# Kernel optimization log

Measured on AMD Instinct MI355X. Metric: run time of the kernel, lower is better.

## Reference

```python
import jax, jax.numpy as jnp
import numpy as np
from jax import lax

# Module config (matches init_kwargs)
C_IN, C_OUT, D_STATE = 512, 256, 16
D_INNER = 2 * C_OUT          # canonical Mamba expand=2
DT_RANK = C_OUT // 16        # ceil(256/16) = 16
D_CONV = 4
BN_EPS = 1e-5


def setup_inputs() -> dict:
    key = jax.random.key(0)
    ks = jax.random.split(key, 16)
    s = 0.02
    B, H, W = 8, 64, 64
    inp = {
        "x": jax.random.normal(ks[0], (B, C_IN, H, W), jnp.float32),
        # lateral 1x1 conv
        "lateral_w": jax.random.normal(ks[1], (C_OUT, C_IN), jnp.float32) * s,
        "lateral_b": jnp.zeros((C_OUT,), jnp.float32),
        # mamba block params
        "in_proj_w": jax.random.normal(ks[2], (2 * D_INNER, C_OUT), jnp.float32) * s,
        "conv1d_w": jax.random.normal(ks[3], (D_INNER, D_CONV), jnp.float32) * s,
        "conv1d_b": jnp.zeros((D_INNER,), jnp.float32),
        "x_proj_w": jax.random.normal(ks[4], (DT_RANK + 2 * D_STATE, D_INNER), jnp.float32) * s,
        "dt_proj_w": jax.random.normal(ks[5], (D_INNER, DT_RANK), jnp.float32) * s,
        "dt_proj_b": jnp.full((D_INNER,), -4.0, jnp.float32),  # softplus -> small dt
        "A_log": jnp.log(jnp.broadcast_to(jnp.arange(1, D_STATE + 1, dtype=jnp.float32), (D_INNER, D_STATE))),  # S4D-real init
        "D_param": jnp.ones((D_INNER,), jnp.float32),
        "out_proj_w": jax.random.normal(ks[6], (C_OUT, D_INNER), jnp.float32) * s,
        # refine: 3x3 conv + BN (eval) + ReLU
        "refine_w": jax.random.normal(ks[7], (C_OUT, C_OUT, 3, 3), jnp.float32) * s,
        "refine_b": jnp.zeros((C_OUT,), jnp.float32),
        "bn_gamma": jnp.ones((C_OUT,), jnp.float32),
        "bn_beta": jnp.zeros((C_OUT,), jnp.float32),
        "bn_mean": jnp.zeros((C_OUT,), jnp.float32),
        "bn_var": jnp.ones((C_OUT,), jnp.float32),
    }
    return inp


def _silu(v):
    return v * jax.nn.sigmoid(v)


def _mamba(u, in_proj_w, conv1d_w, conv1d_b, x_proj_w, dt_proj_w, dt_proj_b,
           A_log, D_param, out_proj_w):
    """Canonical Mamba block on u: (B, L, D) -> (B, L, D)."""
    B, L, D = u.shape
    xz = jnp.einsum('bld,ed->ble', u, in_proj_w)            # (B,L,2*d_inner)
    xm, z = jnp.split(xz, 2, axis=-1)
    # causal depthwise conv1d over L
    xc = xm.transpose(0, 2, 1)                               # (B,d_inner,L)
    xc = lax.conv_general_dilated(xc, conv1d_w[:, None, :], (1,),
                                  [(D_CONV - 1, 0)],
                                  feature_group_count=D_INNER)
    xc = _silu(xc + conv1d_b[None, :, None]).transpose(0, 2, 1)  # (B,L,d_inner)
    proj = jnp.einsum('bld,ed->ble', xc, x_proj_w)           # (B,L,dt_rank+2*N)
    dt_r = proj[..., :DT_RANK]
    B_ssm = proj[..., DT_RANK:DT_RANK + D_STATE]             # (B,L,N)
    C_ssm = proj[..., DT_RANK + D_STATE:]                    # (B,L,N)
    dt = jax.nn.softplus(jnp.einsum('blr,dr->bld', dt_r, dt_proj_w) + dt_proj_b)
    A = -jnp.exp(A_log)                                      # (d_inner,N)

    def step(h, inputs):
        dt_t, B_t, C_t, x_t = inputs                         # (B,d), (B,N), (B,N), (B,d)
        dA = jnp.exp(dt_t[..., None] * A)                    # (B,d,N)
        h = dA * h + dt_t[..., None] * B_t[:, None, :] * x_t[..., None]
        y = jnp.einsum('bdn,bn->bd', h, C_t)
        return h, y

    xs = (dt.transpose(1, 0, 2), B_ssm.transpose(1, 0, 2),
          C_ssm.transpose(1, 0, 2), xc.transpose(1, 0, 2))
    h0 = jnp.zeros((B, D_INNER, D_STATE), u.dtype)
    _, ys = lax.scan(step, h0, xs)                           # (L,B,d_inner)
    y = ys.transpose(1, 0, 2) + xc * D_param
    y = y * _silu(z)
    return jnp.einsum('ble,de->bld', y, out_proj_w)          # (B,L,D)


def reference(x, lateral_w, lateral_b, in_proj_w, conv1d_w, conv1d_b, x_proj_w,
              dt_proj_w, dt_proj_b, A_log, D_param, out_proj_w, refine_w,
              refine_b, bn_gamma, bn_beta, bn_mean, bn_var):
    B, _, H, W = x.shape
    # lateral 1x1 conv
    xl = jnp.einsum('oi,bihw->bohw', lateral_w, x) + lateral_b[None, :, None, None]
    # mamba on flattened spatial sequence, residual add
    u = xl.reshape(B, C_OUT, H * W).transpose(0, 2, 1)        # (B,L,C)
    m = _mamba(u, in_proj_w, conv1d_w, conv1d_b, x_proj_w, dt_proj_w,
               dt_proj_b, A_log, D_param, out_proj_w)
    xr = xl + m.transpose(0, 2, 1).reshape(B, C_OUT, H, W)
    # refine: 3x3 conv + BN(eval) + ReLU
    r = lax.conv_general_dilated(xr, refine_w, (1, 1), [(1, 1), (1, 1)])
    r = r + refine_b[None, :, None, None]
    inv = bn_gamma / jnp.sqrt(bn_var + BN_EPS)
    r = (r - bn_mean[None, :, None, None]) * inv[None, :, None, None] + bn_beta[None, :, None, None]
    return jax.nn.relu(r)
```

## Files before the change

kernel.cpp:

```cpp
#include <hip/hip_runtime.h>
#include <math.h>

#define NB   8
#define CIN  512
#define COUT 256
#define DIN  512
#define LHW  4096
#define NCHK 128
#define CHL  32
#define PW   66
#define PPOS (PW*PW)

typedef __attribute__((ext_vector_type(8))) short bf16x8;
typedef __attribute__((ext_vector_type(4))) float f32x4;

__device__ __forceinline__ float siluf(float v)  { return v / (1.f + __expf(-v)); }
__device__ __forceinline__ float splusf(float v) {
  return fmaxf(v, 0.f) + __logf(1.f + __expf(-fabsf(v)));
}

__device__ __forceinline__ unsigned short f2b(float f) {
  union { float f; unsigned u; } v; v.f = f;
  unsigned r = v.u + 0x7fff + ((v.u >> 16) & 1);
  return (unsigned short)(r >> 16);
}
__device__ __forceinline__ float b2f(unsigned int u) {
  union { unsigned u; float f; } v; v.u = (u & 0xffffu) << 16; return v.f;
}

__device__ __forceinline__ void gload16(const unsigned short* g, unsigned short* l) {
  __builtin_amdgcn_global_load_lds(
      (const __attribute__((address_space(1))) unsigned int*)g,
      (__attribute__((address_space(3))) unsigned int*)l, 16, 0, 0);
}

#define WO1 131072
#define WO2 393216
#define WO3 425984
#define WO4 557056
#define WO5 1146880
__global__ __launch_bounds__(256)
void k_wprep(const float* __restrict__ lw, const float* __restrict__ ipw,
             const float* __restrict__ xpw, const float* __restrict__ opw,
             const float* __restrict__ rw, const float* __restrict__ dtpw,
             unsigned short* __restrict__ wb, unsigned short* __restrict__ wfb) {
  const int i = blockIdx.x * 256 + threadIdx.x;
  if (i < WO1)      wb[i] = f2b(lw[i]);
  else if (i < WO2) wb[i] = f2b(ipw[i - WO1]);
  else if (i < WO3) {
    const int j = i - WO2, row = j >> 9, col = j & 511;
    wb[i] = (row < 48) ? f2b(xpw[row * 512 + col]) : (unsigned short)0;
  }
  else if (i < WO4) wb[i] = f2b(opw[i - WO3]);
  else if (i < WO5) {
    const int j = i - WO4, o = j / 2304, kk = j % 2304;
    const int tap = kk >> 8, ch = kk & 255;
    wb[i] = f2b(rw[(o * 256 + ch) * 9 + tap]);
  }
  else {
    const int j = i - WO5, row = j >> 9, e = j & 511;
    float v = 0.f;
    if (row < 512) {
#pragma unroll
      for (int r = 0; r < 16; ++r)
        v = fmaf(dtpw[row * 16 + r], xpw[r * 512 + e], v);
    } else if (row < 560) {
      v = xpw[(row - 512) * 512 + e];
    }
    wfb[j] = f2b(v);
  }
}

__global__ __launch_bounds__(256)
void k_xpose(const float* __restrict__ x, unsigned short* __restrict__ xt) {
  __shared__ unsigned short Ts[64][80];
  const int b  = blockIdx.z;
  const int k0 = blockIdx.y * 64;
  const int l0 = blockIdx.x * 64;
  const int t  = threadIdx.x;
  const int tx = t & 15, ty = t >> 4;
#pragma unroll
  for (int r = 0; r < 4; ++r) {
    const int k = ty + r * 16;
    float4 v = *(const float4*)(x + ((size_t)b * CIN + k0 + k) * LHW + l0 + tx * 4);
    Ts[tx*4+0][k] = f2b(v.x);
    Ts[tx*4+1][k] = f2b(v.y);
    Ts[tx*4+2][k] = f2b(v.z);
    Ts[tx*4+3][k] = f2b(v.w);
  }
  __syncthreads();
  const int lr = t >> 2, kc = (t & 3) * 16;
  unsigned short* dst = xt + ((size_t)b * LHW + l0 + lr) * CIN + k0 + kc;
  *(uint4*)dst       = *(const uint4*)&Ts[lr][kc];
  *(uint4*)(dst + 8) = *(const uint4*)&Ts[lr][kc + 8];
}

template<int RSA, int RSB, int KTOT>
__device__ __forceinline__ void gemm_loop_128(
    const unsigned short* __restrict__ Ab, const unsigned short* __restrict__ Bb,
    unsigned short (&As)[2][4096], unsigned short (&Bs)[2][4096],
    int t, f32x4 acc[4][4]) {
  const int w = t >> 6, lane = t & 63;
  const int wm = w >> 1, wn = w & 1;
  const int arow = t >> 2;
  const int acol = (((t & 3) ^ ((t >> 3) & 3))) * 8;
  const int fr = lane & 15;
  const int g8 = ((lane >> 4) * 8) ^ (((fr >> 1) & 3) * 8);
  for (int k0 = 0; k0 < KTOT; k0 += 64) {
    __syncthreads();
    gload16(Ab + (size_t)arow * RSA + k0 + acol,             &As[0][w * 512]);
    gload16(Ab + (size_t)(64 + arow) * RSA + k0 + acol,      &As[0][2048 + w*512]);
    gload16(Bb + (size_t)arow * RSB + k0 + acol,             &Bs[0][w * 512]);
    gload16(Bb + (size_t)(64 + arow) * RSB + k0 + acol,      &Bs[0][2048 + w*512]);
    gload16(Ab + (size_t)arow * RSA + k0 + 32 + acol,        &As[1][w * 512]);
    gload16(Ab + (size_t)(64 + arow) * RSA + k0 + 32 + acol, &As[1][2048 + w*512]);
    gload16(Bb + (size_t)arow * RSB + k0 + 32 + acol,        &Bs[1][w * 512]);
    gload16(Bb + (size_t)(64 + arow) * RSB + k0 + 32 + acol, &Bs[1][2048 + w*512]);
    __syncthreads();
#pragma unroll
    for (int h = 0; h < 2; ++h) {
      bf16x8 af[4], bf[4];
#pragma unroll
      for (int f = 0; f < 4; ++f) {
        af[f] = *(const bf16x8*)&As[h][(wm*64 + f*16 + fr) * 32 + g8];
        bf[f] = *(const bf16x8*)&Bs[h][(wn*64 + f*16 + fr) * 32 + g8];
      }
#pragma unroll
      for (int i = 0; i < 4; ++i)
#pragma unroll
        for (int j = 0; j < 4; ++j)
          acc[i][j] = __builtin_amdgcn_mfma_f32_16x16x32_bf16(af[i], bf[j], acc[i][j], 0, 0, 0);
    }
  }
}

__global__ __launch_bounds__(256)
void k_lat_mfma(const unsigned short* __restrict__ xt, const unsigned short* __restrict__ lwb,
                const float* __restrict__ lb, unsigned short* __restrict__ ub) {
  __shared__ __align__(16) unsigned short As[2][4096], Bs[2][4096];
  const int t = threadIdx.x, lane = t & 63, w = t >> 6;
  const int wm = w >> 1, wn = w & 1;
  const int b = blockIdx.z, m0 = blockIdx.y * 128, n0 = blockIdx.x * 128;
  f32x4 acc[4][4] = {};
  gemm_loop_128<512, 512, 512>(xt + ((size_t)b * LHW + m0) * 512,
                               lwb + (size_t)n0 * 512, As, Bs, t, acc);
  const int fr = lane & 15, q4 = (lane >> 4) * 4;
#pragma unroll
  for (int i = 0; i < 4; ++i) {
    const int l = m0 + wm*64 + i*16 + q4;
#pragma unroll
    for (int j = 0; j < 4; ++j) {
      const int o = n0 + wn*64 + j*16 + fr;
      const float bias = lb[o];
      unsigned short* dst = ub + ((size_t)b * LHW + l) * COUT + o;
#pragma unroll
      for (int q = 0; q < 4; ++q)
        dst[(size_t)q * COUT] = f2b(acc[i][j][q] + bias);
    }
  }
}

__global__ __launch_bounds__(256)
void k_inproj_mfma(const unsigned short* __restrict__ ub, const unsigned short* __restrict__ ipwb,
                   unsigned short* __restrict__ xm_b, unsigned short* __restrict__ zsb) {
  __shared__ __align__(16) unsigned short As[2][4096], Bs[2][4096];
  const int t = threadIdx.x, lane = t & 63, w = t >> 6;
  const int wm = w >> 1, wn = w & 1;
  const int b = blockIdx.z, m0 = blockIdx.y * 128, n0 = blockIdx.x * 128;
  f32x4 acc[4][4] = {};
  gemm_loop_128<256, 256, 256>(ub + ((size_t)b * LHW + m0) * 256,
                               ipwb + (size_t)n0 * 256, As, Bs, t, acc);
  const int fr = lane & 15, q4 = (lane >> 4) * 4;
  const bool isz = (n0 >= 512);
#pragma unroll
  for (int i = 0; i < 4; ++i) {
    const int l = m0 + wm*64 + i*16 + q4;
#pragma unroll
    for (int j = 0; j < 4; ++j) {
      const int e = n0 + wn*64 + j*16 + fr;
      if (isz) {
        unsigned short* dst = zsb + ((size_t)b * LHW + l) * DIN + (e - 512);
#pragma unroll
        for (int q = 0; q < 4; ++q)
          dst[(size_t)q * DIN] = f2b(siluf(acc[i][j][q]));
      } else {
        unsigned short* dst = xm_b + ((size_t)b * LHW + l) * DIN + e;
#pragma unroll
        for (int q = 0; q < 4; ++q)
          dst[(size_t)q * DIN] = f2b(acc[i][j][q]);
      }
    }
  }
}

__global__ __launch_bounds__(256)
void k_conv1d(const unsigned short* __restrict__ xm_b, const float* __restrict__ cw,
              const float* __restrict__ cb, unsigned short* __restrict__ xc_b) {
  const int tid = blockIdx.x * 256 + threadIdx.x;
  const int e8 = tid & 63;
  const int lg = tid >> 6;
  const int l0 = (lg & 511) * 8;
  const int b  = lg >> 9;
  const int e0 = e8 * 8;
  float bias[8];
  *(float4*)&bias[0] = *(const float4*)(cb + e0);
  *(float4*)&bias[4] = *(const float4*)(cb + e0 + 4);
  float wv[8][4];
#pragma unroll
  for (int q = 0; q < 8; ++q) {
    float4 w4 = *(const float4*)(cw + (e0 + q) * 4);
    wv[q][0] = w4.x; wv[q][1] = w4.y; wv[q][2] = w4.z; wv[q][3] = w4.w;
  }
  const unsigned short* base = xm_b + ((size_t)b * LHW + l0) * DIN + e0;
  uint4 rows[11];
  const uint4 z4 = make_uint4(0u, 0u, 0u, 0u);
#pragma unroll
  for (int r = 0; r < 11; ++r) {
    const int ll = r - 3;
    rows[r] = (l0 + ll >= 0) ? *(const uint4*)(base + (ptrdiff_t)ll * DIN) : z4;
  }
  unsigned short* outb = xc_b + ((size_t)b * LHW + l0) * DIN + e0;
#pragma unroll
  for (int j = 0; j < 8; ++j) {
    float acc[8];
#pragma unroll
    for (int q = 0; q < 8; ++q) acc[q] = bias[q];
#pragma unroll
    for (int k = 0; k < 4; ++k) {
      const uint4 raw = rows[j + k];
      acc[0] = fmaf(b2f(raw.x),       wv[0][k], acc[0]);
      acc[1] = fmaf(b2f(raw.x >> 16), wv[1][k], acc[1]);
      acc[2] = fmaf(b2f(raw.y),       wv[2][k], acc[2]);
      acc[3] = fmaf(b2f(raw.y >> 16), wv[3][k], acc[3]);
      acc[4] = fmaf(b2f(raw.z),       wv[4][k], acc[4]);
      acc[5] = fmaf(b2f(raw.z >> 16), wv[5][k], acc[5]);
      acc[6] = fmaf(b2f(raw.w),       wv[6][k], acc[6]);
      acc[7] = fmaf(b2f(raw.w >> 16), wv[7][k], acc[7]);
    }
    uint4 o;
    o.x = (unsigned)f2b(siluf(acc[0])) | ((unsigned)f2b(siluf(acc[1])) << 16);
    o.y = (unsigned)f2b(siluf(acc[2])) | ((unsigned)f2b(siluf(acc[3])) << 16);
    o.z = (unsigned)f2b(siluf(acc[4])) | ((unsigned)f2b(siluf(acc[5])) << 16);
    o.w = (unsigned)f2b(siluf(acc[6])) | ((unsigned)f2b(siluf(acc[7])) << 16);
    *(uint4*)(outb + (size_t)j * DIN) = o;
  }
}

__global__ __launch_bounds__(256)
void k_xdt_mfma(const unsigned short* __restrict__ xc_b, const unsigned short* __restrict__ wfb,
                const float* __restrict__ dtpb,
                unsigned short* __restrict__ dtb, float* __restrict__ proj) {
  __shared__ __align__(16) unsigned short As[2][4096], Bs[2][4096];
  const int t = threadIdx.x, lane = t & 63, w = t >> 6;
  const int wm = w >> 1, wn = w & 1;
  const int b = blockIdx.z, m0 = blockIdx.x * 128, n0 = blockIdx.y * 128;
  f32x4 acc[4][4] = {};
  gemm_loop_128<512, 512, 512>(xc_b + ((size_t)b * LHW + m0) * 512,
                               wfb + (size_t)n0 * 512, As, Bs, t, acc);
  const int fr = lane & 15, q4 = (lane >> 4) * 4;
#pragma unroll
  for (int i = 0; i < 4; ++i) {
    const int l = m0 + wm*64 + i*16 + q4;
#pragma unroll
    for (int j = 0; j < 4; ++j) {
      const int c = n0 + wn*64 + j*16 + fr;
      if (c < 512) {
        const float bias = dtpb[c];
        unsigned short* dst = dtb + ((size_t)b * LHW + l) * 512 + c;
#pragma unroll
        for (int q = 0; q < 4; ++q)
          dst[(size_t)q * 512] = f2b(splusf(acc[i][j][q] + bias));
      } else if (c < 560) {
        float* dst = proj + ((size_t)b * LHW + l) * 48 + (c - 512);
#pragma unroll
        for (int q = 0; q < 4; ++q)
          dst[(size_t)q * 48] = acc[i][j][q];
      }
    }
  }
}

__global__ __launch_bounds__(512, 4)
void k_scanA(const float* __restrict__ proj, const unsigned short* __restrict__ dtb,
             const unsigned short* __restrict__ xc_b,
             const float* __restrict__ A_log, float* __restrict__ PS) {
  __shared__ float prs[CHL * 16];
  const int bx = blockIdx.x;
  const int b = bx >> 7, c = bx & 127;
  const int d = threadIdx.x;
  const size_t rbase = (size_t)b * LHW + c * CHL;
  for (int i = d; i < CHL * 4; i += 512) {
    const int row = i >> 2, c4 = i & 3;
    *(float4*)&prs[row * 16 + c4 * 4] = *(const float4*)(proj + (rbase + row) * 48 + 16 + c4 * 4);
  }
  float An[16], h[16];
#pragma unroll
  for (int q = 0; q < 4; ++q) {
    float4 a4 = *(const float4*)(A_log + d*16 + q*4);
    An[q*4+0] = -__expf(a4.x); An[q*4+1] = -__expf(a4.y);
    An[q*4+2] = -__expf(a4.z); An[q*4+3] = -__expf(a4.w);
  }
#pragma unroll
  for (int n = 0; n < 16; ++n) h[n] = 0.f;
  const float An0 = An[0];
  bool lin = true;
#pragma unroll
  for (int n = 1; n < 16; ++n)
    lin = lin && (fabsf(An[n] - (n + 1) * An0) <= 1e-4f * fabsf(An[n]));
  float sdt = 0.f;
  const unsigned short* dt0 = dtb + rbase * 512 + d;
  const unsigned short* xc0 = xc_b + rbase * DIN + d;
  __syncthreads();
  for (int i = 0; i < CHL; ++i) {
    const float dt = b2f(dt0[(size_t)i * 512]);
    sdt += dt;
    const float dtx = dt * b2f(xc0[(size_t)i * DIN]);
    float dA[16];
    if (lin) {
      const float e1 = __expf(dt * An0);
      const float e2 = e1 * e1, e3 = e2 * e1, e4 = e2 * e2;
      dA[0] = e1; dA[1] = e2; dA[2] = e3; dA[3] = e4;
#pragma unroll
      for (int n = 4; n < 16; ++n) dA[n] = dA[n-4] * e4;
    } else {
#pragma unroll
      for (int n = 0; n < 16; ++n) dA[n] = __expf(dt * An[n]);
    }
    const float* pr = &prs[i * 16];
#pragma unroll
    for (int q = 0; q < 4; ++q) {
      float4 B4 = *(const float4*)(pr + q*4);
      h[q*4+0] = fmaf(dA[q*4+0], h[q*4+0], dtx * B4.x);
      h[q*4+1] = fmaf(dA[q*4+1], h[q*4+1], dtx * B4.y);
      h[q*4+2] = fmaf(dA[q*4+2], h[q*4+2], dtx * B4.z);
      h[q*4+3] = fmaf(dA[q*4+3], h[q*4+3], dtx * B4.w);
    }
  }
  float* o = PS + ((size_t)bx * 512 + d) * 32;
#pragma unroll
  for (int q = 0; q < 4; ++q)
    *(float4*)(o + q*4) = make_float4(__expf(sdt*An[q*4+0]), __expf(sdt*An[q*4+1]),
                                      __expf(sdt*An[q*4+2]), __expf(sdt*An[q*4+3]));
#pragma unroll
  for (int q = 0; q < 4; ++q)
    *(float4*)(o + 16 + q*4) = make_float4(h[q*4], h[q*4+1], h[q*4+2], h[q*4+3]);
}

__global__ __launch_bounds__(256)
void k_scanB(const float* __restrict__ PS, float* __restrict__ hst) {
  const int tid = blockIdx.x * 256 + threadIdx.x;
  const int n = tid & 15;
  const int d = (tid >> 4) & 511;
  const int b = tid >> 13;
  float h = 0.f;
  for (int c = 0; c < NCHK; ++c) {
    const size_t idx = (size_t)((b*NCHK + c)*512 + d);
    hst[idx*16 + n] = h;
    h = PS[idx*32 + n] * h + PS[idx*32 + 16 + n];
  }
}

__global__ __launch_bounds__(512, 4)
void k_scanC(const float* __restrict__ proj, const unsigned short* __restrict__ dtb,
             const unsigned short* __restrict__ xc_b,
             const unsigned short* __restrict__ zsb, const float* __restrict__ hst,
             const float* __restrict__ A_log, const float* __restrict__ Dpar,
             unsigned short* __restrict__ ydata) {
  __shared__ float prs[CHL * 32];
  const int bx = blockIdx.x;
  const int b = bx >> 7, c = bx & 127;
  const int d = threadIdx.x;
  const size_t rbase = (size_t)b * LHW + c * CHL;
  for (int i = d; i < CHL * 8; i += 512) {
    const int row = i >> 3, c4 = i & 7;
    *(float4*)&prs[row * 32 + c4 * 4] = *(const float4*)(proj + (rbase + row) * 48 + 16 + c4 * 4);
  }
  float An[16], h[16];
#pragma unroll
  for (int q = 0; q < 4; ++q) {
    float4 a4 = *(const float4*)(A_log + d*16 + q*4);
    An[q*4+0] = -__expf(a4.x); An[q*4+1] = -__expf(a4.y);
    An[q*4+2] = -__expf(a4.z); An[q*4+3] = -__expf(a4.w);
  }
#pragma unroll
  for (int q = 0; q < 4; ++q) {
    float4 h4 = *(const float4*)(hst + ((size_t)bx * 512 + d) * 16 + q*4);
    h[q*4+0] = h4.x; h[q*4+1] = h4.y; h[q*4+2] = h4.z; h[q*4+3] = h4.w;
  }
  const float An0 = An[0];
  bool lin = true;
#pragma unroll
  for (int n = 1; n < 16; ++n)
    lin = lin && (fabsf(An[n] - (n + 1) * An0) <= 1e-4f * fabsf(An[n]));
  const float dp = Dpar[d];
  const unsigned short* dt0 = dtb + rbase * 512 + d;
  const unsigned short* xc0 = xc_b + rbase * DIN + d;
  const unsigned short* zs0 = zsb + rbase * DIN + d;
  unsigned short* y0 = ydata + rbase * DIN + d;
  __syncthreads();
  for (int i = 0; i < CHL; ++i) {
    const float dt = b2f(dt0[(size_t)i * 512]);
    const float xt = b2f(xc0[(size_t)i * DIN]);
    const float zv = b2f(zs0[(size_t)i * DIN]);
    const float dtx = dt * xt;
    float dA[16];
    if (lin) {
      const float e1 = __expf(dt * An0);
      const float e2 = e1 * e1, e3 = e2 * e1, e4 = e2 * e2;
      dA[0] = e1; dA[1] = e2; dA[2] = e3; dA[3] = e4;
#pragma unroll
      for (int n = 4; n < 16; ++n) dA[n] = dA[n-4] * e4;
    } else {
#pragma unroll
      for (int n = 0; n < 16; ++n) dA[n] = __expf(dt * An[n]);
    }
    const float* pr = &prs[i * 32];
    float y0a = 0.f, y1a = 0.f, y2a = 0.f, y3a = 0.f;
#pragma unroll
    for (int q = 0; q < 4; ++q) {
      float4 B4 = *(const float4*)(pr + q*4);
      float4 C4 = *(const float4*)(pr + 16 + q*4);
      h[q*4+0] = fmaf(dA[q*4+0], h[q*4+0], dtx * B4.x);
      h[q*4+1] = fmaf(dA[q*4+1], h[q*4+1], dtx * B4.y);
      h[q*4+2] = fmaf(dA[q*4+2], h[q*4+2], dtx * B4.z);
      h[q*4+3] = fmaf(dA[q*4+3], h[q*4+3], dtx * B4.w);
      y0a = fmaf(h[q*4+0], C4.x, y0a);
      y1a = fmaf(h[q*4+1], C4.y, y1a);
      y2a = fmaf(h[q*4+2], C4.z, y2a);
      y3a = fmaf(h[q*4+3], C4.w, y3a);
    }
    const float y = (y0a + y1a) + (y2a + y3a);
    y0[(size_t)i * DIN] = f2b((y + xt * dp) * zv);
  }
}

__global__ __launch_bounds__(256)
void k_outproj_mfma(const unsigned short* __restrict__ ydata, const unsigned short* __restrict__ opwb,
                    const unsigned short* __restrict__ ub, unsigned short* __restrict__ xrp) {
  __shared__ __align__(16) unsigned short As[2][4096], Bs[2][4096];
  const int t = threadIdx.x, lane = t & 63, w = t >> 6;
  const int wm = w >> 1, wn = w & 1;
  const int b = blockIdx.z, m0 = blockIdx.y * 128, n0 = blockIdx.x * 128;
  f32x4 acc[4][4] = {};
  gemm_loop_128<512, 512, 512>(ydata + ((size_t)b * LHW + m0) * 512,
                               opwb + (size_t)n0 * 512, As, Bs, t, acc);
  const int fr = lane & 15, q4 = (lane >> 4) * 4;
#pragma unroll
  for (int i = 0; i < 4; ++i) {
    const int lbase = m0 + wm*64 + i*16 + q4;
#pragma unroll
    for (int q = 0; q < 4; ++q) {
      const int l = lbase + q;
      const int pos = ((l >> 6) + 1) * PW + (l & 63) + 1;
#pragma unroll
      for (int j = 0; j < 4; ++j) {
        const int o = n0 + wn*64 + j*16 + fr;
        const float r = b2f(ub[((size_t)b * LHW + l) * COUT + o]);
        xrp[((size_t)b * PPOS + pos) * COUT + o] = f2b(acc[i][j][q] + r);
      }
    }
  }
}

__global__ __launch_bounds__(256)
void k_refine_mfma(const unsigned short* __restrict__ Aw,
                   const unsigned short* __restrict__ xrp,
                   const float* __restrict__ rb, const float* __restrict__ bng,
                   const float* __restrict__ bnb, const float* __restrict__ bnm,
                   const float* __restrict__ bnv, float* __restrict__ out) {
  __shared__ __align__(16) unsigned short As[4][4096], Bs[4][4096];
  const int t = threadIdx.x;
  const int lane = t & 63;
  const int w = t >> 6;
  const int wm = w >> 1, wn = w & 1;
  const int b  = blockIdx.z;
  const int m0 = blockIdx.y * 128;
  const int n0 = blockIdx.x * 128;
  const int y0 = n0 >> 6;
  const unsigned short* xb = xrp + (size_t)b * PPOS * COUT;
  const int arow = t >> 2;
  const int acol = (((t & 3) ^ ((t >> 3) & 3))) * 8;
  const int fr = lane & 15;
  const int g8 = ((lane >> 4) * 8) ^ (((fr >> 1) & 3) * 8);

#define RF_STAGE(ks, buf) {                                                            \
    const int tap_ = (ks) >> 3;                                                        \
    const int i0_  = ((ks) & 7) * 32;                                                  \
    const int ky_  = tap_ / 3, kx_ = tap_ - ky_ * 3;                                   \
    const int k0_  = tap_ * 256 + i0_;                                                 \
    const unsigned short* ga_ = Aw + (size_t)(m0 + arow) * 2304 + k0_ + acol;          \
    const unsigned short* gb_ = xb + ((size_t)((y0 + ky_) * PW + kx_ + arow)) * COUT + i0_ + acol; \
    gload16(ga_,              &As[buf][w * 512]);                                      \
    gload16(ga_ + 64 * 2304,  &As[buf][2048 + w * 512]);                               \
    gload16(gb_,              &Bs[buf][w * 512]);                                      \
    gload16(gb_ + PW * COUT,  &Bs[buf][2048 + w * 512]);                               \
  }

  f32x4 acc[4][4] = {};
  for (int ks = 0; ks < 72; ks += 4) {
    __syncthreads();
    RF_STAGE(ks, 0);
    RF_STAGE(ks + 1, 1);
    RF_STAGE(ks + 2, 2);
    RF_STAGE(ks + 3, 3);
    __syncthreads();
#pragma unroll
    for (int h = 0; h < 4; ++h) {
      bf16x8 af[4], bfr[4];
#pragma unroll
      for (int f = 0; f < 4; ++f) {
        af[f]  = *(const bf16x8*)&As[h][(wm*64 + f*16 + fr) * 32 + g8];
        bfr[f] = *(const bf16x8*)&Bs[h][(wn*64 + f*16 + fr) * 32 + g8];
      }
#pragma unroll
      for (int i = 0; i < 4; ++i)
#pragma unroll
        for (int j = 0; j < 4; ++j)
          acc[i][j] = __builtin_amdgcn_mfma_f32_16x16x32_bf16(af[i], bfr[j], acc[i][j], 0, 0, 0);
    }
  }
#undef RF_STAGE
  const int q4 = (lane >> 4) * 4;
#pragma unroll
  for (int i = 0; i < 4; ++i) {
    const int obase = m0 + wm*64 + i*16 + q4;
#pragma unroll
    for (int q = 0; q < 4; ++q) {
      const int o = obase + q;
      const float inv = bng[o] * rsqrtf(bnv[o] + 1e-5f);
      const float sh  = (rb[o] - bnm[o]) * inv + bnb[o];
      float* orow = out + ((size_t)b * COUT + o) * LHW + n0 + wn*64 + fr;
#pragma unroll
      for (int j = 0; j < 4; ++j)
        orow[j*16] = fmaxf(fmaf(acc[i][j][q], inv, sh), 0.f);
    }
  }
}

extern "C" void kernel_launch(void* const* d_in, const int* in_sizes, int n_in,
                              void* d_out, int out_size, void* d_ws, size_t ws_size,
                              hipStream_t stream) {
  const float* x    = (const float*)d_in[0];
  const float* lw   = (const float*)d_in[1];
  const float* lb   = (const float*)d_in[2];
  const float* ipw  = (const float*)d_in[3];
  const float* cw   = (const float*)d_in[4];
  const float* cb   = (const float*)d_in[5];
  const float* xpw  = (const float*)d_in[6];
  const float* dtpw = (const float*)d_in[7];
  const float* dtpb = (const float*)d_in[8];
  const float* Alog = (const float*)d_in[9];
  const float* Dpar = (const float*)d_in[10];
  const float* opw  = (const float*)d_in[11];
  const float* rw   = (const float*)d_in[12];
  const float* rb   = (const float*)d_in[13];
  const float* bng  = (const float*)d_in[14];
  const float* bnb  = (const float*)d_in[15];
  const float* bnm  = (const float*)d_in[16];
  const float* bnv  = (const float*)d_in[17];
  float* out = (float*)d_out;

  float* ws = (float*)d_ws;
  unsigned short* ub   = (unsigned short*)ws;
  unsigned short* xt   = (unsigned short*)(ws + 4194304);
  unsigned short* xm_b = (unsigned short*)(ws + 12582912);
  unsigned short* xc_b = (unsigned short*)(ws + 20971520);
  unsigned short* zsb  = (unsigned short*)(ws + 29360128);
  float* proj = ws + 37748736;
  float* PS   = ws + 39321600;
  float* hst  = ws + 56098816;
  unsigned short* wb  = (unsigned short*)(ws + 64487424);
  unsigned short* wfb = (unsigned short*)(ws + 65060864);
  unsigned short* lwb  = wb;
  unsigned short* ipwb = wb + WO1;
  unsigned short* opwb = wb + WO3;
  unsigned short* Aw   = wb + WO4;
  unsigned short* ydata = xm_b;
  unsigned short* dtb   = xt;
  unsigned short* xrp   = xt;

  k_wprep<<<dim3(5760), 256, 0, stream>>>(lw, ipw, xpw, opw, rw, dtpw, wb, wfb);
  k_xpose<<<dim3(64, 8, 8), 256, 0, stream>>>(x, xt);
  k_lat_mfma<<<dim3(2, 32, 8), 256, 0, stream>>>(xt, lwb, lb, ub);
  k_inproj_mfma<<<dim3(8, 32, 8), 256, 0, stream>>>(ub, ipwb, xm_b, zsb);
  k_conv1d<<<dim3(1024), 256, 0, stream>>>(xm_b, cw, cb, xc_b);
  k_xdt_mfma<<<dim3(32, 5, 8), 256, 0, stream>>>(xc_b, wfb, dtpb, dtb, proj);
  k_scanA<<<dim3(NB * NCHK), 512, 0, stream>>>(proj, dtb, xc_b, Alog, PS);
  k_scanB<<<dim3(256), 256, 0, stream>>>(PS, hst);
  k_scanC<<<dim3(NB * NCHK), 512, 0, stream>>>(proj, dtb, xc_b, zsb, hst, Alog, Dpar, ydata);
  hipMemsetAsync(xrp, 0, (size_t)NB * PPOS * COUT * sizeof(unsigned short), stream);
  k_outproj_mfma<<<dim3(2, 32, 8), 256, 0, stream>>>(ydata, opwb, ub, xrp);
  k_refine_mfma<<<dim3(32, 2, 8), 256, 0, stream>>>(Aw, xrp, rb, bng, bnb, bnm, bnv, out);
}
```

Measured before the change: 344.6 us.

## Split scan state across thread pairs and recompute chunk decay in scanB

The chunked selective-scan kernels now assign each channel to two threads, each holding eight of the sixteen state elements, with twice as many blocks. In scanC the partial output dot products are combined with a lane shuffle and only one thread of each pair writes. scanA no longer stores the per-chunk decay products; it stores only the chunk's summed dt, and scanB recomputes the decay with an exp, which roughly halves that intermediate's traffic. The aim is more parallelism and lower register pressure in the sequential scan, in exchange for duplicated dt/x/z loads per pair and extra shuffles.

```diff
diff --git a/kernel.cpp b/kernel.cpp
--- a/kernel.cpp
+++ b/kernel.cpp
@@ -282,31 +282,34 @@
 
 __global__ __launch_bounds__(512, 4)
 void k_scanA(const float* __restrict__ proj, const unsigned short* __restrict__ dtb,
-             const unsigned short* __restrict__ xc_b,
-             const float* __restrict__ A_log, float* __restrict__ PS) {
+             const unsigned short* __restrict__ xc_b, const float* __restrict__ A_log,
+             float* __restrict__ Sst, float* __restrict__ SDT) {
   __shared__ float prs[CHL * 16];
-  const int bx = blockIdx.x;
-  const int b = bx >> 7, c = bx & 127;
-  const int d = threadIdx.x;
+  const int chunkid = blockIdx.x >> 1;
+  const int dg = blockIdx.x & 1;
+  const int b = chunkid >> 7, c = chunkid & 127;
+  const int t = threadIdx.x;
+  const int d = dg * 256 + (t >> 1);
+  const int hf = t & 1;
   const size_t rbase = (size_t)b * LHW + c * CHL;
-  for (int i = d; i < CHL * 4; i += 512) {
+  for (int i = t; i < CHL * 4; i += 512) {
     const int row = i >> 2, c4 = i & 3;
     *(float4*)&prs[row * 16 + c4 * 4] = *(const float4*)(proj + (rbase + row) * 48 + 16 + c4 * 4);
   }
-  float An[16], h[16];
-#pragma unroll
-  for (int q = 0; q < 4; ++q) {
-    float4 a4 = *(const float4*)(A_log + d*16 + q*4);
-    An[q*4+0] = -__expf(a4.x); An[q*4+1] = -__expf(a4.y);
-    An[q*4+2] = -__expf(a4.z); An[q*4+3] = -__expf(a4.w);
-  }
-#pragma unroll
-  for (int n = 0; n < 16; ++n) h[n] = 0.f;
-  const float An0 = An[0];
+  float An[8], h[8];
+  {
+    float4 a0 = *(const float4*)(A_log + d*16 + hf*8);
+    float4 a1 = *(const float4*)(A_log + d*16 + hf*8 + 4);
+    An[0]=-__expf(a0.x); An[1]=-__expf(a0.y); An[2]=-__expf(a0.z); An[3]=-__expf(a0.w);
+    An[4]=-__expf(a1.x); An[5]=-__expf(a1.y); An[6]=-__expf(a1.z); An[7]=-__expf(a1.w);
+  }
+  const float An0g = -__expf(A_log[d * 16]);
+#pragma unroll
+  for (int k = 0; k < 8; ++k) h[k] = 0.f;
   bool lin = true;
 #pragma unroll
-  for (int n = 1; n < 16; ++n)
-    lin = lin && (fabsf(An[n] - (n + 1) * An0) <= 1e-4f * fabsf(An[n]));
+  for (int k = 0; k < 8; ++k)
+    lin = lin && (fabsf(An[k] - (hf*8 + k + 1) * An0g) <= 1e-4f * fabsf(An[k]));
   float sdt = 0.f;
   const unsigned short* dt0 = dtb + rbase * 512 + d;
   const unsigned short* xc0 = xc_b + rbase * DIN + d;
@@ -315,48 +318,45 @@
     const float dt = b2f(dt0[(size_t)i * 512]);
     sdt += dt;
     const float dtx = dt * b2f(xc0[(size_t)i * DIN]);
-    float dA[16];
+    float dA[8];
     if (lin) {
-      const float e1 = __expf(dt * An0);
-      const float e2 = e1 * e1, e3 = e2 * e1, e4 = e2 * e2;
-      dA[0] = e1; dA[1] = e2; dA[2] = e3; dA[3] = e4;
-#pragma unroll
-      for (int n = 4; n < 16; ++n) dA[n] = dA[n-4] * e4;
+      const float e1 = __expf(dt * An0g);
+      const float e2 = e1*e1, e3 = e2*e1, e4 = e2*e2;
+      const float e8 = e4*e4;
+      const float st = e1 * (hf ? e8 : 1.f);
+      dA[0]=st; dA[1]=st*e1; dA[2]=st*e2; dA[3]=st*e3;
+      dA[4]=dA[0]*e4; dA[5]=dA[1]*e4; dA[6]=dA[2]*e4; dA[7]=dA[3]*e4;
     } else {
 #pragma unroll
-      for (int n = 0; n < 16; ++n) dA[n] = __expf(dt * An[n]);
-    }
-    const float* pr = &prs[i * 16];
-#pragma unroll
-    for (int q = 0; q < 4; ++q) {
-      float4 B4 = *(const float4*)(pr + q*4);
-      h[q*4+0] = fmaf(dA[q*4+0], h[q*4+0], dtx * B4.x);
-      h[q*4+1] = fmaf(dA[q*4+1], h[q*4+1], dtx * B4.y);
-      h[q*4+2] = fmaf(dA[q*4+2], h[q*4+2], dtx * B4.z);
-      h[q*4+3] = fmaf(dA[q*4+3], h[q*4+3], dtx * B4.w);
-    }
-  }
-  float* o = PS + ((size_t)bx * 512 + d) * 32;
-#pragma unroll
-  for (int q = 0; q < 4; ++q)
-    *(float4*)(o + q*4) = make_float4(__expf(sdt*An[q*4+0]), __expf(sdt*An[q*4+1]),
-                                      __expf(sdt*An[q*4+2]), __expf(sdt*An[q*4+3]));
-#pragma unroll
-  for (int q = 0; q < 4; ++q)
-    *(float4*)(o + 16 + q*4) = make_float4(h[q*4], h[q*4+1], h[q*4+2], h[q*4+3]);
-}
-
-__global__ __launch_bounds__(256)
-void k_scanB(const float* __restrict__ PS, float* __restrict__ hst) {
+      for (int k = 0; k < 8; ++k) dA[k] = __expf(dt * An[k]);
+    }
+    const float* pr = &prs[i * 16 + hf * 8];
+    float4 B0 = *(const float4*)pr;
+    float4 B1 = *(const float4*)(pr + 4);
+    h[0]=fmaf(dA[0],h[0],dtx*B0.x); h[1]=fmaf(dA[1],h[1],dtx*B0.y);
+    h[2]=fmaf(dA[2],h[2],dtx*B0.z); h[3]=fmaf(dA[3],h[3],dtx*B0.w);
+    h[4]=fmaf(dA[4],h[4],dtx*B1.x); h[5]=fmaf(dA[5],h[5],dtx*B1.y);
+    h[6]=fmaf(dA[6],h[6],dtx*B1.z); h[7]=fmaf(dA[7],h[7],dtx*B1.w);
+  }
+  float* o = Sst + ((size_t)chunkid * 512 + d) * 16 + hf * 8;
+  *(float4*)o       = make_float4(h[0], h[1], h[2], h[3]);
+  *(float4*)(o + 4) = make_float4(h[4], h[5], h[6], h[7]);
+  if (!hf) SDT[(size_t)chunkid * 512 + d] = sdt;
+}
+
+__global__ __launch_bounds__(256)
+void k_scanB(const float* __restrict__ Sst, const float* __restrict__ SDT,
+             const float* __restrict__ A_log, float* __restrict__ hst) {
   const int tid = blockIdx.x * 256 + threadIdx.x;
   const int n = tid & 15;
   const int d = (tid >> 4) & 511;
   const int b = tid >> 13;
+  const float An = -__expf(A_log[d * 16 + n]);
   float h = 0.f;
   for (int c = 0; c < NCHK; ++c) {
     const size_t idx = (size_t)((b*NCHK + c)*512 + d);
     hst[idx*16 + n] = h;
-    h = PS[idx*32 + n] * h + PS[idx*32 + 16 + n];
+    h = __expf(SDT[idx] * An) * h + Sst[idx*16 + n];
   }
 }
 
@@ -367,31 +367,36 @@
              const float* __restrict__ A_log, const float* __restrict__ Dpar,
              unsigned short* __restrict__ ydata) {
   __shared__ float prs[CHL * 32];
-  const int bx = blockIdx.x;
-  const int b = bx >> 7, c = bx & 127;
-  const int d = threadIdx.x;
+  const int chunkid = blockIdx.x >> 1;
+  const int dg = blockIdx.x & 1;
+  const int b = chunkid >> 7, c = chunkid & 127;
+  const int t = threadIdx.x;
+  const int d = dg * 256 + (t >> 1);
+  const int hf = t & 1;
   const size_t rbase = (size_t)b * LHW + c * CHL;
-  for (int i = d; i < CHL * 8; i += 512) {
+  for (int i = t; i < CHL * 8; i += 512) {
     const int row = i >> 3, c4 = i & 7;
     *(float4*)&prs[row * 32 + c4 * 4] = *(const float4*)(proj + (rbase + row) * 48 + 16 + c4 * 4);
   }
-  float An[16], h[16];
-#pragma unroll
-  for (int q = 0; q < 4; ++q) {
-    float4 a4 = *(const float4*)(A_log + d*16 + q*4);
-    An[q*4+0] = -__expf(a4.x); An[q*4+1] = -__expf(a4.y);
-    An[q*4+2] = -__expf(a4.z); An[q*4+3] = -__expf(a4.w);
-  }
-#pragma unroll
-  for (int q = 0; q < 4; ++q) {
-    float4 h4 = *(const float4*)(hst + ((size_t)bx * 512 + d) * 16 + q*4);
-    h[q*4+0] = h4.x; h[q*4+1] = h4.y; h[q*4+2] = h4.z; h[q*4+3] = h4.w;
-  }
-  const float An0 = An[0];
+  float An[8], h[8];
+  {
+    float4 a0 = *(const float4*)(A_log + d*16 + hf*8);
+    float4 a1 = *(const float4*)(A_log + d*16 + hf*8 + 4);
+    An[0]=-__expf(a0.x); An[1]=-__expf(a0.y); An[2]=-__expf(a0.z); An[3]=-__expf(a0.w);
+    An[4]=-__expf(a1.x); An[5]=-__expf(a1.y); An[6]=-__expf(a1.z); An[7]=-__expf(a1.w);
+  }
+  const float An0g = -__expf(A_log[d * 16]);
+  {
+    const float* hsrc = hst + ((size_t)chunkid * 512 + d) * 16 + hf * 8;
+    float4 h0 = *(const float4*)hsrc;
+    float4 h1 = *(const float4*)(hsrc + 4);
+    h[0]=h0.x; h[1]=h0.y; h[2]=h0.z; h[3]=h0.w;
+    h[4]=h1.x; h[5]=h1.y; h[6]=h1.z; h[7]=h1.w;
+  }
   bool lin = true;
 #pragma unroll
-  for (int n = 1; n < 16; ++n)
-    lin = lin && (fabsf(An[n] - (n + 1) * An0) <= 1e-4f * fabsf(An[n]));
+  for (int k = 0; k < 8; ++k)
+    lin = lin && (fabsf(An[k] - (hf*8 + k + 1) * An0g) <= 1e-4f * fabsf(An[k]));
   const float dp = Dpar[d];
   const unsigned short* dt0 = dtb + rbase * 512 + d;
   const unsigned short* xc0 = xc_b + rbase * DIN + d;
@@ -403,34 +408,38 @@
     const float xt = b2f(xc0[(size_t)i * DIN]);
     const float zv = b2f(zs0[(size_t)i * DIN]);
     const float dtx = dt * xt;
-    float dA[16];
+    float dA[8];
     if (lin) {
-      const float e1 = __expf(dt * An0);
-      const float e2 = e1 * e1, e3 = e2 * e1, e4 = e2 * e2;
-      dA[0] = e1; dA[1] = e2; dA[2] = e3; dA[3] = e4;
-#pragma unroll
-      for (int n = 4; n < 16; ++n) dA[n] = dA[n-4] * e4;
+      const float e1 = __expf(dt * An0g);
+      const float e2 = e1*e1, e3 = e2*e1, e4 = e2*e2;
+      const float e8 = e4*e4;
+      const float st = e1 * (hf ? e8 : 1.f);
+      dA[0]=st; dA[1]=st*e1; dA[2]=st*e2; dA[3]=st*e3;
+      dA[4]=dA[0]*e4; dA[5]=dA[1]*e4; dA[6]=dA[2]*e4; dA[7]=dA[3]*e4;
     } else {
 #pragma unroll
-      for (int n = 0; n < 16; ++n) dA[n] = __expf(dt * An[n]);
+      for (int k = 0; k < 8; ++k) dA[k] = __expf(dt * An[k]);
     }
     const float* pr = &prs[i * 32];
-    float y0a = 0.f, y1a = 0.f, y2a = 0.f, y3a = 0.f;
-#pragma unroll
-    for (int q = 0; q < 4; ++q) {
-      float4 B4 = *(const float4*)(pr + q*4);
-      float4 C4 = *(const float4*)(pr + 16 + q*4);
-      h[q*4+0] = fmaf(dA[q*4+0], h[q*4+0], dtx * B4.x);
-      h[q*4+1] = fmaf(dA[q*4+1], h[q*4+1], dtx * B4.y);
-      h[q*4+2] = fmaf(dA[q*4+2], h[q*4+2], dtx * B4.z);
-      h[q*4+3] = fmaf(dA[q*4+3], h[q*4+3], dtx * B4.w);
-      y0a = fmaf(h[q*4+0], C4.x, y0a);
-      y1a = fmaf(h[q*4+1], C4.y, y1a);
-      y2a = fmaf(h[q*4+2], C4.z, y2a);
-      y3a = fmaf(h[q*4+3], C4.w, y3a);
-    }
-    const float y = (y0a + y1a) + (y2a + y3a);
-    y0[(size_t)i * DIN] = f2b((y + xt * dp) * zv);
+    float4 B0 = *(const float4*)(pr + hf * 8);
+    float4 B1 = *(const float4*)(pr + hf * 8 + 4);
+    float4 C0 = *(const float4*)(pr + 16 + hf * 8);
+    float4 C1 = *(const float4*)(pr + 16 + hf * 8 + 4);
+    float ya = 0.f, yb = 0.f;
+    h[0]=fmaf(dA[0],h[0],dtx*B0.x); ya=fmaf(h[0],C0.x,ya);
+    h[1]=fmaf(dA[1],h[1],dtx*B0.y); yb=fmaf(h[1],C0.y,yb);
+    h[2]=fmaf(dA[2],h[2],dtx*B0.z); ya=fmaf(h[2],C0.z,ya);
+    h[3]=fmaf(dA[3],h[3],dtx*B0.w); yb=fmaf(h[3],C0.w,yb);
+    h[4]=fmaf(dA[4],h[4],dtx*B1.x); ya=fmaf(h[4],C1.x,ya);
+    h[5]=fmaf(dA[5],h[5],dtx*B1.y); yb=fmaf(h[5],C1.y,yb);
+    h[6]=fmaf(dA[6],h[6],dtx*B1.z); ya=fmaf(h[6],C1.z,ya);
+    h[7]=fmaf(dA[7],h[7],dtx*B1.w); yb=fmaf(h[7],C1.w,yb);
+    float y = ya + yb;
+    y += __shfl_xor(y, 1);
+    if (!hf) {
+      const float ov = (y + xt * dp) * zv;
+      y0[(size_t)i * DIN] = f2b(ov);
+    }
   }
 }
 
@@ -567,8 +576,9 @@
   unsigned short* xc_b = (unsigned short*)(ws + 20971520);
   unsigned short* zsb  = (unsigned short*)(ws + 29360128);
   float* proj = ws + 37748736;
-  float* PS   = ws + 39321600;
-  float* hst  = ws + 56098816;
+  float* Sst  = ws + 39321600;
+  float* SDT  = ws + 47710208;
+  float* hst  = ws + 48234496;
   unsigned short* wb  = (unsigned short*)(ws + 64487424);
   unsigned short* wfb = (unsigned short*)(ws + 65060864);
   unsigned short* lwb  = wb;
@@ -585,9 +595,9 @@
   k_inproj_mfma<<<dim3(8, 32, 8), 256, 0, stream>>>(ub, ipwb, xm_b, zsb);
   k_conv1d<<<dim3(1024), 256, 0, stream>>>(xm_b, cw, cb, xc_b);
   k_xdt_mfma<<<dim3(32, 5, 8), 256, 0, stream>>>(xc_b, wfb, dtpb, dtb, proj);
-  k_scanA<<<dim3(NB * NCHK), 512, 0, stream>>>(proj, dtb, xc_b, Alog, PS);
-  k_scanB<<<dim3(256), 256, 0, stream>>>(PS, hst);
-  k_scanC<<<dim3(NB * NCHK), 512, 0, stream>>>(proj, dtb, xc_b, zsb, hst, Alog, Dpar, ydata);
+  k_scanA<<<dim3(NB * NCHK * 2), 512, 0, stream>>>(proj, dtb, xc_b, Alog, Sst, SDT);
+  k_scanB<<<dim3(256), 256, 0, stream>>>(Sst, SDT, Alog, hst);
+  k_scanC<<<dim3(NB * NCHK * 2), 512, 0, stream>>>(proj, dtb, xc_b, zsb, hst, Alog, Dpar, ydata);
   hipMemsetAsync(xrp, 0, (size_t)NB * PPOS * COUT * sizeof(unsigned short), stream);
   k_outproj_mfma<<<dim3(2, 32, 8), 256, 0, stream>>>(ydata, opwb, ub, xrp);
   k_refine_mfma<<<dim3(32, 2, 8), 256, 0, stream>>>(Aw, xrp, rb, bng, bnb, bnm, bnv, out);
```

Result: no change. 349.0 us (+1.3%).

## Use packed FP32 math in scan kernels and store chunk dt-sums instead of decay

Applied to the files above, without the earlier changes.

The scan recurrences in scanA and scanC now use v_pk_fma_f32/v_pk_mul_f32 inline asm on float pairs, roughly halving the VALU instruction count for the 16-state update and output dot product. scanA no longer writes per-chunk decay factors; it stores only the chunk dt sum, and scanB recomputes exp(sdt*A) itself. This cuts scanA's global write traffic and PS buffer size. In exchange scanB does an extra exp per step, and the inline asm may limit compiler scheduling.

```diff
diff --git a/kernel.cpp b/kernel.cpp
--- a/kernel.cpp
+++ b/kernel.cpp
@@ -13,6 +13,7 @@
 
 typedef __attribute__((ext_vector_type(8))) short bf16x8;
 typedef __attribute__((ext_vector_type(4))) float f32x4;
+typedef __attribute__((ext_vector_type(2))) float f32x2;
 
 __device__ __forceinline__ float siluf(float v)  { return v / (1.f + __expf(-v)); }
 __device__ __forceinline__ float splusf(float v) {
@@ -26,6 +27,17 @@
 }
 __device__ __forceinline__ float b2f(unsigned int u) {
   union { unsigned u; float f; } v; v.u = (u & 0xffffu) << 16; return v.f;
+}
+
+__device__ __forceinline__ f32x2 pk_fma(f32x2 a, f32x2 b, f32x2 c) {
+  f32x2 d;
+  asm("v_pk_fma_f32 %0, %1, %2, %3" : "=v"(d) : "v"(a), "v"(b), "v"(c));
+  return d;
+}
+__device__ __forceinline__ f32x2 pk_mul(f32x2 a, f32x2 b) {
+  f32x2 d;
+  asm("v_pk_mul_f32 %0, %1, %2" : "=v"(d) : "v"(a), "v"(b));
+  return d;
 }
 
 __device__ __forceinline__ void gload16(const unsigned short* g, unsigned short* l) {
@@ -282,8 +294,8 @@
 
 __global__ __launch_bounds__(512, 4)
 void k_scanA(const float* __restrict__ proj, const unsigned short* __restrict__ dtb,
-             const unsigned short* __restrict__ xc_b,
-             const float* __restrict__ A_log, float* __restrict__ PS) {
+             const unsigned short* __restrict__ xc_b, const float* __restrict__ A_log,
+             float* __restrict__ Sst, float* __restrict__ SDT) {
   __shared__ float prs[CHL * 16];
   const int bx = blockIdx.x;
   const int b = bx >> 7, c = bx & 127;
@@ -293,15 +305,16 @@
     const int row = i >> 2, c4 = i & 3;
     *(float4*)&prs[row * 16 + c4 * 4] = *(const float4*)(proj + (rbase + row) * 48 + 16 + c4 * 4);
   }
-  float An[16], h[16];
+  float An[16];
 #pragma unroll
   for (int q = 0; q < 4; ++q) {
     float4 a4 = *(const float4*)(A_log + d*16 + q*4);
     An[q*4+0] = -__expf(a4.x); An[q*4+1] = -__expf(a4.y);
     An[q*4+2] = -__expf(a4.z); An[q*4+3] = -__expf(a4.w);
   }
-#pragma unroll
-  for (int n = 0; n < 16; ++n) h[n] = 0.f;
+  f32x2 h2[8];
+#pragma unroll
+  for (int k = 0; k < 8; ++k) h2[k] = (f32x2){0.f, 0.f};
   const float An0 = An[0];
   bool lin = true;
 #pragma unroll
@@ -315,48 +328,50 @@
     const float dt = b2f(dt0[(size_t)i * 512]);
     sdt += dt;
     const float dtx = dt * b2f(xc0[(size_t)i * DIN]);
-    float dA[16];
+    const f32x2 dtx2 = (f32x2){dtx, dtx};
+    f32x2 dA2[8];
     if (lin) {
       const float e1 = __expf(dt * An0);
-      const float e2 = e1 * e1, e3 = e2 * e1, e4 = e2 * e2;
-      dA[0] = e1; dA[1] = e2; dA[2] = e3; dA[3] = e4;
-#pragma unroll
-      for (int n = 4; n < 16; ++n) dA[n] = dA[n-4] * e4;
+      const float e2 = e1*e1, e3 = e2*e1, e4 = e2*e2, e8 = e4*e4;
+      const f32x2 e4v = (f32x2){e4, e4}, e8v = (f32x2){e8, e8};
+      dA2[0] = (f32x2){e1, e2};
+      dA2[1] = (f32x2){e3, e4};
+      dA2[2] = pk_mul(dA2[0], e4v);
+      dA2[3] = pk_mul(dA2[1], e4v);
+      dA2[4] = pk_mul(dA2[0], e8v);
+      dA2[5] = pk_mul(dA2[1], e8v);
+      dA2[6] = pk_mul(dA2[2], e8v);
+      dA2[7] = pk_mul(dA2[3], e8v);
     } else {
 #pragma unroll
-      for (int n = 0; n < 16; ++n) dA[n] = __expf(dt * An[n]);
-    }
-    const float* pr = &prs[i * 16];
-#pragma unroll
-    for (int q = 0; q < 4; ++q) {
-      float4 B4 = *(const float4*)(pr + q*4);
-      h[q*4+0] = fmaf(dA[q*4+0], h[q*4+0], dtx * B4.x);
-      h[q*4+1] = fmaf(dA[q*4+1], h[q*4+1], dtx * B4.y);
-      h[q*4+2] = fmaf(dA[q*4+2], h[q*4+2], dtx * B4.z);
-      h[q*4+3] = fmaf(dA[q*4+3], h[q*4+3], dtx * B4.w);
-    }
-  }
-  float* o = PS + ((size_t)bx * 512 + d) * 32;
-#pragma unroll
-  for (int q = 0; q < 4; ++q)
-    *(float4*)(o + q*4) = make_float4(__expf(sdt*An[q*4+0]), __expf(sdt*An[q*4+1]),
-                                      __expf(sdt*An[q*4+2]), __expf(sdt*An[q*4+3]));
-#pragma unroll
-  for (int q = 0; q < 4; ++q)
-    *(float4*)(o + 16 + q*4) = make_float4(h[q*4], h[q*4+1], h[q*4+2], h[q*4+3]);
-}
-
-__global__ __launch_bounds__(256)
-void k_scanB(const float* __restrict__ PS, float* __restrict__ hst) {
+      for (int k = 0; k < 8; ++k)
+        dA2[k] = (f32x2){__expf(dt * An[2*k]), __expf(dt * An[2*k+1])};
+    }
+    const f32x2* B2 = (const f32x2*)&prs[i * 16];
+#pragma unroll
+    for (int k = 0; k < 8; ++k)
+      h2[k] = pk_fma(dA2[k], h2[k], pk_mul(dtx2, B2[k]));
+  }
+  float* o = Sst + ((size_t)bx * 512 + d) * 16;
+#pragma unroll
+  for (int k = 0; k < 4; ++k)
+    *(float4*)(o + k*4) = make_float4(h2[2*k].x, h2[2*k].y, h2[2*k+1].x, h2[2*k+1].y);
+  SDT[(size_t)bx * 512 + d] = sdt;
+}
+
+__global__ __launch_bounds__(256)
+void k_scanB(const float* __restrict__ Sst, const float* __restrict__ SDT,
+             const float* __restrict__ A_log, float* __restrict__ hst) {
   const int tid = blockIdx.x * 256 + threadIdx.x;
   const int n = tid & 15;
   const int d = (tid >> 4) & 511;
   const int b = tid >> 13;
+  const float An = -__expf(A_log[d * 16 + n]);
   float h = 0.f;
   for (int c = 0; c < NCHK; ++c) {
     const size_t idx = (size_t)((b*NCHK + c)*512 + d);
     hst[idx*16 + n] = h;
-    h = PS[idx*32 + n] * h + PS[idx*32 + 16 + n];
+    h = __expf(SDT[idx] * An) * h + Sst[idx*16 + n];
   }
 }
 
@@ -375,17 +390,19 @@
     const int row = i >> 3, c4 = i & 7;
     *(float4*)&prs[row * 32 + c4 * 4] = *(const float4*)(proj + (rbase + row) * 48 + 16 + c4 * 4);
   }
-  float An[16], h[16];
+  float An[16];
 #pragma unroll
   for (int q = 0; q < 4; ++q) {
     float4 a4 = *(const float4*)(A_log + d*16 + q*4);
     An[q*4+0] = -__expf(a4.x); An[q*4+1] = -__expf(a4.y);
     An[q*4+2] = -__expf(a4.z); An[q*4+3] = -__expf(a4.w);
   }
-#pragma unroll
-  for (int q = 0; q < 4; ++q) {
-    float4 h4 = *(const float4*)(hst + ((size_t)bx * 512 + d) * 16 + q*4);
-    h[q*4+0] = h4.x; h[q*4+1] = h4.y; h[q*4+2] = h4.z; h[q*4+3] = h4.w;
+  f32x2 h2[8];
+  {
+    const float* hsrc = hst + ((size_t)bx * 512 + d) * 16;
+#pragma unroll
+    for (int k = 0; k < 8; ++k)
+      h2[k] = *(const f32x2*)(hsrc + 2*k);
   }
   const float An0 = An[0];
   bool lin = true;
@@ -403,34 +420,37 @@
     const float xt = b2f(xc0[(size_t)i * DIN]);
     const float zv = b2f(zs0[(size_t)i * DIN]);
     const float dtx = dt * xt;
-    float dA[16];
+    const f32x2 dtx2 = (f32x2){dtx, dtx};
+    f32x2 dA2[8];
     if (lin) {
       const float e1 = __expf(dt * An0);
-      const float e2 = e1 * e1, e3 = e2 * e1, e4 = e2 * e2;
-      dA[0] = e1; dA[1] = e2; dA[2] = e3; dA[3] = e4;
-#pragma unroll
-      for (int n = 4; n < 16; ++n) dA[n] = dA[n-4] * e4;
+      const float e2 = e1*e1, e3 = e2*e1, e4 = e2*e2, e8 = e4*e4;
+      const f32x2 e4v = (f32x2){e4, e4}, e8v = (f32x2){e8, e8};
+      dA2[0] = (f32x2){e1, e2};
+      dA2[1] = (f32x2){e3, e4};
+      dA2[2] = pk_mul(dA2[0], e4v);
+      dA2[3] = pk_mul(dA2[1], e4v);
+      dA2[4] = pk_mul(dA2[0], e8v);
+      dA2[5] = pk_mul(dA2[1], e8v);
+      dA2[6] = pk_mul(dA2[2], e8v);
+      dA2[7] = pk_mul(dA2[3], e8v);
     } else {
 #pragma unroll
-      for (int n = 0; n < 16; ++n) dA[n] = __expf(dt * An[n]);
-    }
-    const float* pr = &prs[i * 32];
-    float y0a = 0.f, y1a = 0.f, y2a = 0.f, y3a = 0.f;
-#pragma unroll
-    for (int q = 0; q < 4; ++q) {
-      float4 B4 = *(const float4*)(pr + q*4);
-      float4 C4 = *(const float4*)(pr + 16 + q*4);
-      h[q*4+0] = fmaf(dA[q*4+0], h[q*4+0], dtx * B4.x);
-      h[q*4+1] = fmaf(dA[q*4+1], h[q*4+1], dtx * B4.y);
-      h[q*4+2] = fmaf(dA[q*4+2], h[q*4+2], dtx * B4.z);
-      h[q*4+3] = fmaf(dA[q*4+3], h[q*4+3], dtx * B4.w);
-      y0a = fmaf(h[q*4+0], C4.x, y0a);
-      y1a = fmaf(h[q*4+1], C4.y, y1a);
-      y2a = fmaf(h[q*4+2], C4.z, y2a);
-      y3a = fmaf(h[q*4+3], C4.w, y3a);
-    }
-    const float y = (y0a + y1a) + (y2a + y3a);
-    y0[(size_t)i * DIN] = f2b((y + xt * dp) * zv);
+      for (int k = 0; k < 8; ++k)
+        dA2[k] = (f32x2){__expf(dt * An[2*k]), __expf(dt * An[2*k+1])};
+    }
+    const f32x2* B2 = (const f32x2*)&prs[i * 32];
+    const f32x2* C2 = (const f32x2*)&prs[i * 32 + 16];
+    f32x2 ya = (f32x2){0.f, 0.f}, yb = (f32x2){0.f, 0.f};
+#pragma unroll
+    for (int k = 0; k < 8; ++k) {
+      h2[k] = pk_fma(dA2[k], h2[k], pk_mul(dtx2, B2[k]));
+      if (k & 1) yb = pk_fma(h2[k], C2[k], yb);
+      else       ya = pk_fma(h2[k], C2[k], ya);
+    }
+    const float y = (ya.x + ya.y) + (yb.x + yb.y);
+    const float ov = (y + xt * dp) * zv;
+    y0[(size_t)i * DIN] = f2b(ov);
   }
 }
 
@@ -567,8 +587,9 @@
   unsigned short* xc_b = (unsigned short*)(ws + 20971520);
   unsigned short* zsb  = (unsigned short*)(ws + 29360128);
   float* proj = ws + 37748736;
-  float* PS   = ws + 39321600;
-  float* hst  = ws + 56098816;
+  float* Sst  = ws + 39321600;
+  float* SDT  = ws + 47710208;
+  float* hst  = ws + 48234496;
   unsigned short* wb  = (unsigned short*)(ws + 64487424);
   unsigned short* wfb = (unsigned short*)(ws + 65060864);
   unsigned short* lwb  = wb;
@@ -585,8 +606,8 @@
   k_inproj_mfma<<<dim3(8, 32, 8), 256, 0, stream>>>(ub, ipwb, xm_b, zsb);
   k_conv1d<<<dim3(1024), 256, 0, stream>>>(xm_b, cw, cb, xc_b);
   k_xdt_mfma<<<dim3(32, 5, 8), 256, 0, stream>>>(xc_b, wfb, dtpb, dtb, proj);
-  k_scanA<<<dim3(NB * NCHK), 512, 0, stream>>>(proj, dtb, xc_b, Alog, PS);
-  k_scanB<<<dim3(256), 256, 0, stream>>>(PS, hst);
+  k_scanA<<<dim3(NB * NCHK), 512, 0, stream>>>(proj, dtb, xc_b, Alog, Sst, SDT);
+  k_scanB<<<dim3(256), 256, 0, stream>>>(Sst, SDT, Alog, hst);
   k_scanC<<<dim3(NB * NCHK), 512, 0, stream>>>(proj, dtb, xc_b, zsb, hst, Alog, Dpar, ydata);
   hipMemsetAsync(xrp, 0, (size_t)NB * PPOS * COUT * sizeof(unsigned short), stream);
   k_outproj_mfma<<<dim3(2, 32, 8), 256, 0, stream>>>(ydata, opwb, ub, xrp);
```

Result: no change. 343.4 us (-0.3%).
